# Kernel optimization log

Hardware: AMD Instinct MI355X
Metric: run time of the kernel (lower is better)

The kernel has to match this reference:

```python
import jax, jax.numpy as jnp
import numpy as np

HIDDEN = 1024
HEADS = 16
HEAD_DIM = HIDDEN // HEADS


def setup_inputs() -> dict:
    key = jax.random.key(0)
    ks = jax.random.split(key, 9)
    B, S = 2, 2048
    std = 1.0 / np.sqrt(HIDDEN)
    inp = {
        'hidden_states': jax.random.normal(ks[0], (B, S, HIDDEN), dtype=jnp.float32),
        'attention_mask': jnp.ones((B, S), dtype=jnp.int32),
        'wq': jax.random.normal(ks[1], (HIDDEN, HIDDEN), dtype=jnp.float32) * std,
        'bq': jnp.zeros((HIDDEN,), dtype=jnp.float32),
        'wk': jax.random.normal(ks[2], (HIDDEN, HIDDEN), dtype=jnp.float32) * std,
        'bk': jnp.zeros((HIDDEN,), dtype=jnp.float32),
        'wv': jax.random.normal(ks[3], (HIDDEN, HIDDEN), dtype=jnp.float32) * std,
        'bv': jnp.zeros((HIDDEN,), dtype=jnp.float32),
        'wo': jax.random.normal(ks[4], (HIDDEN, HIDDEN), dtype=jnp.float32) * std,
        'bo': jnp.zeros((HIDDEN,), dtype=jnp.float32),
    }
    return inp


def reference(hidden_states, attention_mask, wq, bq, wk, bk, wv, bv, wo, bo):
    B, S, H = hidden_states.shape
    def heads(x):  # [B,S,H] -> [B,nh,S,hd]
        return x.reshape(B, S, HEADS, HEAD_DIM).transpose(0, 2, 1, 3)
    q = heads(hidden_states @ wq + bq)
    k = heads(hidden_states @ wk + bk)
    v = heads(hidden_states @ wv + bv)
    scores = jnp.einsum('bhqd,bhkd->bhqk', q, k) / np.sqrt(HEAD_DIM).astype(np.float32)
    causal = jnp.tril(jnp.ones((S, S), dtype=bool))  # True = keep
    keep = causal[None, None] & (attention_mask[:, None, None, :] != 0)
    scores = jnp.where(keep, scores, -jnp.inf)
    probs = jax.nn.softmax(scores, axis=-1)
    out = jnp.einsum('bhqk,bhkd->bhqd', probs, v)  # [B,nh,S,hd]
    out = out.transpose(0, 2, 1, 3).reshape(B, S, H)
    return out @ wo + bo
```

## Files before the change

### kernel.cpp

```cpp
#include <hip/hip_runtime.h>

#define HID   1024
#define SLEN  2048
#define NHEAD 16
#define HDIM  64
#define SC2L  0.18033688f

typedef unsigned short u16;
typedef _Float16 f16;
using bf16x8 = __attribute__((ext_vector_type(8))) short;
using f16x4  = __attribute__((ext_vector_type(4))) f16;
using f32x4  = __attribute__((ext_vector_type(4))) float;

typedef __attribute__((address_space(1))) void gvoid;
typedef __attribute__((address_space(3))) void lvoid;

__device__ __forceinline__ u16 f2bf(float f) {
  union { float f; unsigned u; } v; v.f = f;
  unsigned u = v.u;
  return (u16)((u + 0x7fffu + ((u >> 16) & 1u)) >> 16);
}

__device__ __forceinline__ void async_ld16(const u16* g, u16* l) {
  __builtin_amdgcn_global_load_lds((gvoid*)g, (lvoid*)l, 16, 0, 0);
}

__global__ __launch_bounds__(256) void prep_kernel(const float* __restrict__ x,
                                                   const float* __restrict__ wq,
                                                   const float* __restrict__ wk,
                                                   const float* __restrict__ wv,
                                                   const float* __restrict__ wo,
                                                   u16* __restrict__ xb,
                                                   u16* __restrict__ wt) {
  const int tid = threadIdx.x;
  if (blockIdx.z == 4) {
    const int bid = blockIdx.y * 32 + blockIdx.x;
#pragma unroll
    for (int it = 0; it < 4; ++it) {
      const int i = bid * 1024 + it * 256 + tid;
      float4 v = ((const float4*)x)[i];
      ushort4 o;
      o.x = f2bf(v.x); o.y = f2bf(v.y); o.z = f2bf(v.z); o.w = f2bf(v.w);
      ((ushort4*)xb)[i] = o;
    }
    return;
  }
  const float* src = (blockIdx.z == 0) ? wq : (blockIdx.z == 1) ? wk
                   : (blockIdx.z == 2) ? wv : wo;
  u16* dst = wt + (size_t)blockIdx.z * (HID * HID);
  __shared__ float tile[32][33];
  const int n0 = blockIdx.x * 32, k0 = blockIdx.y * 32;
  const int xx = tid & 31, yy = tid >> 5;
  for (int i = yy; i < 32; i += 8)
    tile[i][xx] = src[(size_t)(k0 + i) * HID + n0 + xx];
  __syncthreads();
  for (int i = yy; i < 32; i += 8)
    dst[(size_t)(n0 + i) * HID + k0 + xx] = f2bf(tile[xx][i]);
}

__global__ __launch_bounds__(256) void gemm_qkv_kernel(const u16* __restrict__ A,
                                                       const u16* __restrict__ Bt,
                                                       const float* __restrict__ bq,
                                                       const float* __restrict__ bk,
                                                       const float* __restrict__ bv,
                                                       u16* __restrict__ Qb,
                                                       u16* __restrict__ Kb,
                                                       u16* __restrict__ VTf) {
  __shared__ u16 smem[8192];
  u16* sA = smem;
  u16* sB = smem + 4096;
  const int tid  = threadIdx.x;
  const int wave = tid >> 6, lane = tid & 63;
  const int quad = lane >> 4, l16 = lane & 15;
  const int n0g = blockIdx.x * 128;
  const int region = blockIdx.x >> 3;
  const int colbase = (blockIdx.x & 7) * 128;
  const int m0 = blockIdx.y * 128;
  const int wm = (wave & 1) * 64, wn = (wave >> 1) * 64;

  f32x4 acc[4][4] = {};
  const int srow = lane >> 2;
  const int scol = (lane & 3) * 8;

  for (int kt = 0; kt < HID; kt += 32) {
    __syncthreads();
    for (int c = wave; c < 8; c += 4) {
      async_ld16(A  + (size_t)(m0  + c * 16 + srow) * HID + kt + scol, &sA[c * 512]);
      async_ld16(Bt + (size_t)(n0g + c * 16 + srow) * HID + kt + scol, &sB[c * 512]);
    }
    __syncthreads();

    bf16x8 af[4], bfr[4];
#pragma unroll
    for (int t = 0; t < 4; ++t) {
      af[t]  = *(const bf16x8*)&sA[(wm + t * 16 + l16) * 32 + quad * 8];
      bfr[t] = *(const bf16x8*)&sB[(wn + t * 16 + l16) * 32 + quad * 8];
    }
#pragma unroll
    for (int mt = 0; mt < 4; ++mt)
#pragma unroll
      for (int nt = 0; nt < 4; ++nt)
        acc[mt][nt] = __builtin_amdgcn_mfma_f32_16x16x32_bf16(af[mt], bfr[nt],
                                                              acc[mt][nt], 0, 0, 0);
  }

  const float* bias = (region == 0) ? bq : (region == 1) ? bk : bv;
  float bvv[4];
#pragma unroll
  for (int nt = 0; nt < 4; ++nt) bvv[nt] = bias[colbase + wn + nt * 16 + l16];

  if (region == 2) {
    const int bb = m0 >> 11;
    const int m0loc = m0 & 2047;
    const int h0 = colbase >> 6;
    u16* T = smem;
#pragma unroll
    for (int h2 = 0; h2 < 2; ++h2) {
      __syncthreads();
      if ((wave >> 1) == h2) {
#pragma unroll
        for (int mt = 0; mt < 4; ++mt)
#pragma unroll
          for (int nt = 0; nt < 4; ++nt)
#pragma unroll
            for (int r = 0; r < 4; ++r) {
              const int sl = (wave & 1) * 64 + mt * 16 + quad * 4 + r;
              const int dl = nt * 16 + l16;
              union { f16 h; u16 u; } cv;
              cv.h = (f16)(acc[mt][nt][r] + bvv[nt]);
              T[dl * 128 + (((sl >> 3) ^ l16) * 8) + (sl & 7)] = cv.u;
            }
      }
      __syncthreads();
      const int d = tid >> 2, sg = (tid & 3) * 4;
      u16* drow = VTf + (size_t)((bb * NHEAD + h0 + h2) * HDIM + d) * SLEN + m0loc;
#pragma unroll
      for (int cc = 0; cc < 4; ++cc) {
        const int cl = sg + cc;
        const int ph = cl ^ (d & 15);
        *(bf16x8*)(drow + cl * 8) = *(const bf16x8*)&T[d * 128 + ph * 8];
      }
    }
    return;
  }

  u16* C = (region == 0) ? Qb : Kb;
#pragma unroll
  for (int mt = 0; mt < 4; ++mt)
#pragma unroll
    for (int r = 0; r < 4; ++r) {
      const int row = m0 + wm + mt * 16 + quad * 4 + r;
#pragma unroll
      for (int nt = 0; nt < 4; ++nt) {
        const int col = colbase + wn + nt * 16 + l16;
        C[(size_t)row * HID + col] = f2bf(acc[mt][nt][r] + bvv[nt]);
      }
    }
}

__global__ __launch_bounds__(256) void gemm_o_kernel(const u16* __restrict__ A,
                                                     const u16* __restrict__ Bt,
                                                     const float* __restrict__ bias,
                                                     float* __restrict__ Cf) {
  __shared__ u16 sA[64 * 32];
  __shared__ u16 sB[128 * 32];
  const int tid  = threadIdx.x;
  const int wave = tid >> 6, lane = tid & 63;
  const int quad = lane >> 4, l16 = lane & 15;
  const int n0 = blockIdx.x * 128;
  const int m0 = blockIdx.y * 64;
  const int wn = wave * 32;

  f32x4 acc[4][2] = {};
  const int srow = lane >> 2;
  const int scol = (lane & 3) * 8;

  for (int kt = 0; kt < HID; kt += 32) {
    __syncthreads();
    for (int c = wave; c < 12; c += 4) {
      if (c < 4) async_ld16(A  + (size_t)(m0 + c * 16 + srow) * HID + kt + scol, &sA[c * 512]);
      else       async_ld16(Bt + (size_t)(n0 + (c - 4) * 16 + srow) * HID + kt + scol,
                            &sB[(c - 4) * 512]);
    }
    __syncthreads();

    bf16x8 af[4], bfr[2];
#pragma unroll
    for (int t = 0; t < 4; ++t)
      af[t] = *(const bf16x8*)&sA[(t * 16 + l16) * 32 + quad * 8];
#pragma unroll
    for (int t = 0; t < 2; ++t)
      bfr[t] = *(const bf16x8*)&sB[(wn + t * 16 + l16) * 32 + quad * 8];
#pragma unroll
    for (int mt = 0; mt < 4; ++mt)
#pragma unroll
      for (int nt = 0; nt < 2; ++nt)
        acc[mt][nt] = __builtin_amdgcn_mfma_f32_16x16x32_bf16(af[mt], bfr[nt],
                                                              acc[mt][nt], 0, 0, 0);
  }

  float bvv[2];
#pragma unroll
  for (int nt = 0; nt < 2; ++nt) bvv[nt] = bias[n0 + wn + nt * 16 + l16];
#pragma unroll
  for (int mt = 0; mt < 4; ++mt)
#pragma unroll
    for (int r = 0; r < 4; ++r) {
      const int row = m0 + mt * 16 + quad * 4 + r;
#pragma unroll
      for (int nt = 0; nt < 2; ++nt)
        Cf[(size_t)row * HID + n0 + wn + nt * 16 + l16] = acc[mt][nt][r] + bvv[nt];
    }
}

__global__ __launch_bounds__(256, 2) void flash_attn_kernel(const u16* __restrict__ Q,
                                                            const u16* __restrict__ K,
                                                            const u16* __restrict__ VT,
                                                            const int* __restrict__ mask,
                                                            u16* __restrict__ O) {
  const int xb = blockIdx.x, h = blockIdx.y, b = blockIdx.z;
  const int tid  = threadIdx.x;
  const int wave = tid >> 6, lane = tid & 63;
  const int quad = lane >> 4, l16 = lane & 15;

  __shared__ alignas(16) char smraw[35840];
  u16*   Ks  = (u16*)smraw;
  u16*   Vt  = (u16*)(smraw + 16384);
  float* Ob0 = (float*)smraw;
  float* Ob1 = (float*)(smraw + 16896);
  float* lb  = (float*)(smraw + 33792);

  const u16* Kh  = K  + (size_t)b * SLEN * HID + h * HDIM;
  const u16* Vth = VT + (size_t)((b * NHEAD + h) * HDIM) * SLEN;

  const int srow8 = lane >> 3;
  const int gch   = (lane & 7) ^ srow8;
  const int rx    = l16 & 7;

  for (int phase = 0; phase < 2; ++phase) {
    const int qt = phase ? (31 - xb) : xb;
    const int q0 = qt * 64;

    bf16x8 qb[4][2];
#pragma unroll
    for (int nt = 0; nt < 4; ++nt) {
      const u16* qp = Q + (size_t)(b * SLEN + q0 + nt * 16 + l16) * HID + h * HDIM + quad * 8;
      qb[nt][0] = *(const bf16x8*)qp;
      qb[nt][1] = *(const bf16x8*)(qp + 32);
    }

    f32x4 oacc[4][4] = {};
    float l_part[4] = {0.f, 0.f, 0.f, 0.f};

    {
      const int r0 = wave * 16 + srow8;
      async_ld16(Kh  + (size_t)r0 * HID + gch * 8,        Ks + wave * 1024);
      async_ld16(Kh  + (size_t)(r0 + 8) * HID + gch * 8,  Ks + wave * 1024 + 512);
      async_ld16(Vth + (size_t)r0 * SLEN + gch * 8,       Vt + wave * 1024);
      async_ld16(Vth + (size_t)(r0 + 8) * SLEN + gch * 8, Vt + wave * 1024 + 512);
    }
    __syncthreads();

    for (int j = 0; j <= qt; ++j) {
      const int buf = j & 1;
      u16* KsB = Ks + buf * 4096;
      u16* VtB = Vt + buf * 4096;

      if (j < qt) {
        const int nb = (buf ^ 1) * 4096;
        const int jn = (j + 1) * 64;
        const int r0 = wave * 16 + srow8;
        async_ld16(Kh  + (size_t)(jn + r0) * HID + gch * 8,       Ks + nb + wave * 1024);
        async_ld16(Kh  + (size_t)(jn + r0 + 8) * HID + gch * 8,   Ks + nb + wave * 1024 + 512);
        async_ld16(Vth + (size_t)r0 * SLEN + jn + gch * 8,        Vt + nb + wave * 1024);
        async_ld16(Vth + (size_t)(r0 + 8) * SLEN + jn + gch * 8,  Vt + nb + wave * 1024 + 512);
      }

      const int4 mi = *(const int4*)(mask + b * SLEN + j * 64 + wave * 16 + quad * 4);
      float map[4];
      map[0] = mi.x ? 0.f : -1e30f;  map[1] = mi.y ? 0.f : -1e30f;
      map[2] = mi.z ? 0.f : -1e30f;  map[3] = mi.w ? 0.f : -1e30f;

      const u16* kp = KsB + (wave * 16 + l16) * 64;
      const int ph0 = quad ^ rx;
      const bf16x8 ka0 = *(const bf16x8*)(kp + ph0 * 8);
      const bf16x8 ka1 = *(const bf16x8*)(kp + (ph0 ^ 4) * 8);

      float p[4][4];
#pragma unroll
      for (int nt = 0; nt < 4; ++nt) {
        f32x4 z = {0.f, 0.f, 0.f, 0.f};
        z = __builtin_amdgcn_mfma_f32_16x16x32_bf16(ka0, qb[nt][0], z, 0, 0, 0);
        z = __builtin_amdgcn_mfma_f32_16x16x32_bf16(ka1, qb[nt][1], z, 0, 0, 0);
#pragma unroll
        for (int r = 0; r < 4; ++r)
          p[nt][r] = exp2f(fmaf(z[r], SC2L, map[r]));
      }
      if (j == qt) {
#pragma unroll
        for (int nt = 0; nt < 4; ++nt)
#pragma unroll
          for (int r = 0; r < 4; ++r)
            if (wave * 16 + quad * 4 + r > nt * 16 + l16) p[nt][r] = 0.f;
      }

      f16x4 pb[4];
#pragma unroll
      for (int nt = 0; nt < 4; ++nt) {
        l_part[nt] += (p[nt][0] + p[nt][1]) + (p[nt][2] + p[nt][3]);
        pb[nt][0] = (f16)p[nt][0]; pb[nt][1] = (f16)p[nt][1];
        pb[nt][2] = (f16)p[nt][2]; pb[nt][3] = (f16)p[nt][3];
      }

      const int phv = (wave * 2 + (quad >> 1)) ^ rx;
      const int vsub = phv * 8 + (quad & 1) * 4;
#pragma unroll
      for (int dt = 0; dt < 4; ++dt) {
        const f16x4 va = *(const f16x4*)(VtB + (dt * 16 + l16) * 64 + vsub);
#pragma unroll
        for (int nt = 0; nt < 4; ++nt)
          oacc[dt][nt] = __builtin_amdgcn_mfma_f32_16x16x16f16(va, pb[nt], oacc[dt][nt], 0, 0, 0);
      }
      __syncthreads();
    }

#pragma unroll
    for (int nt = 0; nt < 4; ++nt) {
      l_part[nt] += __shfl_xor(l_part[nt], 16);
      l_part[nt] += __shfl_xor(l_part[nt], 32);
    }
    if (quad == 0)
#pragma unroll
      for (int nt = 0; nt < 4; ++nt) lb[wave * 64 + nt * 16 + l16] = l_part[nt];

    if ((wave & 1) == 0) {
      float* ob = (wave == 0) ? Ob0 : Ob1;
#pragma unroll
      for (int dt = 0; dt < 4; ++dt)
#pragma unroll
        for (int nt = 0; nt < 4; ++nt)
#pragma unroll
          for (int r = 0; r < 4; ++r)
            ob[(dt * 16 + quad * 4 + r) * 66 + nt * 16 + l16] = oacc[dt][nt][r];
    }
    __syncthreads();
    if (wave & 1) {
      float* ob = (wave == 1) ? Ob0 : Ob1;
#pragma unroll
      for (int dt = 0; dt < 4; ++dt)
#pragma unroll
        for (int nt = 0; nt < 4; ++nt)
#pragma unroll
          for (int r = 0; r < 4; ++r)
            ob[(dt * 16 + quad * 4 + r) * 66 + nt * 16 + l16] += oacc[dt][nt][r];
    }
    __syncthreads();

    {
      const int q  = tid >> 2;
      const int dc = tid & 3;
      const float l = lb[q] + lb[64 + q] + lb[128 + q] + lb[192 + q];
      const float inv = 1.f / l;
      u16 ob[16];
#pragma unroll
      for (int e = 0; e < 16; ++e) {
        const int d = dc * 16 + e;
        ob[e] = f2bf((Ob0[d * 66 + q] + Ob1[d * 66 + q]) * inv);
      }
      u16* op = O + (size_t)(b * SLEN + q0 + q) * HID + h * HDIM + dc * 16;
      *(bf16x8*)op       = *(bf16x8*)&ob[0];
      *(bf16x8*)(op + 8) = *(bf16x8*)&ob[8];
    }
    __syncthreads();
  }
}

extern "C" void kernel_launch(void* const* d_in, const int* in_sizes, int n_in,
                              void* d_out, int out_size, void* d_ws, size_t ws_size,
                              hipStream_t stream) {
  const float* x    = (const float*)d_in[0];
  const int*   mask = (const int*)d_in[1];
  const float* wq   = (const float*)d_in[2];
  const float* bq   = (const float*)d_in[3];
  const float* wk   = (const float*)d_in[4];
  const float* bk   = (const float*)d_in[5];
  const float* wv   = (const float*)d_in[6];
  const float* bv   = (const float*)d_in[7];
  const float* wo   = (const float*)d_in[8];
  const float* bo   = (const float*)d_in[9];
  float* out = (float*)d_out;

  char* ws = (char*)d_ws;
  u16* XBF = (u16*)(ws);
  u16* WT  = (u16*)(ws + (8u  << 20));
  u16* QBF = (u16*)(ws + (16u << 20));
  u16* KBF = (u16*)(ws + (24u << 20));
  u16* VTF = (u16*)(ws + (32u << 20));
  u16* ATT = (u16*)(ws);

  prep_kernel<<<dim3(32, 32, 5), 256, 0, stream>>>(x, wq, wk, wv, wo, XBF, WT);
  gemm_qkv_kernel<<<dim3(24, 32), 256, 0, stream>>>(XBF, WT, bq, bk, bv, QBF, KBF, VTF);
  flash_attn_kernel<<<dim3(16, NHEAD, 2), 256, 0, stream>>>(QBF, KBF, VTF, mask, ATT);
  gemm_o_kernel<<<dim3(8, 64), 256, 0, stream>>>(ATT, WT + (3u << 20), bo, out);
}
```

Baseline: 208.7 us.

## Re-layout V^T into per-wave slabs and drop block barriers in attention loop

The V^T projection output is stored in contiguous 2KB slabs of 16 keys by 64 dims, with an XOR swizzle. This lets each wave async-load exactly the K and V rows it later consumes. Because no wave reads another wave's LDS tiles, the per-iteration __syncthreads is replaced by per-wave s_waitcnt vmcnt waits, and the next tile's mask load is prefetched. This removes cross-wave barrier stalls and gives more contiguous V loads. The cost is reliance on hand-placed waitcnt ordering for async LDS loads.

Result: faster. 199.2 us (-4.6%).

```diff
diff --git a/kernel.cpp b/kernel.cpp
--- a/kernel.cpp
+++ b/kernel.cpp
@@ -133,12 +133,14 @@
       }
       __syncthreads();
       const int d = tid >> 2, sg = (tid & 3) * 4;
-      u16* drow = VTf + (size_t)((bb * NHEAD + h0 + h2) * HDIM + d) * SLEN + m0loc;
+      u16* slab0 = VTf + ((size_t)((bb * NHEAD + h0 + h2) * 128 + (m0loc >> 4))) * 1024;
 #pragma unroll
       for (int cc = 0; cc < 4; ++cc) {
         const int cl = sg + cc;
         const int ph = cl ^ (d & 15);
-        *(bf16x8*)(drow + cl * 8) = *(const bf16x8*)&T[d * 128 + ph * 8];
+        const int slot = (d * 2 + (cl & 1)) ^ ((d >> 2) & 1);
+        *(bf16x8*)(slab0 + (size_t)(cl >> 1) * 1024 + slot * 8)
+            = *(const bf16x8*)&T[d * 128 + ph * 8];
       }
     }
     return;
@@ -231,7 +233,7 @@
   float* lb  = (float*)(smraw + 33792);
 
   const u16* Kh  = K  + (size_t)b * SLEN * HID + h * HDIM;
-  const u16* Vth = VT + (size_t)((b * NHEAD + h) * HDIM) * SLEN;
+  const u16* Vth = VT + (size_t)(b * NHEAD + h) * (128 * 1024);
 
   const int srow8 = lane >> 3;
   const int gch   = (lane & 7) ^ srow8;
@@ -254,29 +256,39 @@
 
     {
       const int r0 = wave * 16 + srow8;
-      async_ld16(Kh  + (size_t)r0 * HID + gch * 8,        Ks + wave * 1024);
-      async_ld16(Kh  + (size_t)(r0 + 8) * HID + gch * 8,  Ks + wave * 1024 + 512);
-      async_ld16(Vth + (size_t)r0 * SLEN + gch * 8,       Vt + wave * 1024);
-      async_ld16(Vth + (size_t)(r0 + 8) * SLEN + gch * 8, Vt + wave * 1024 + 512);
-    }
-    __syncthreads();
+      u16* kd = Ks + wave * 1024;
+      async_ld16(Kh + (size_t)r0 * HID + gch * 8,       kd);
+      async_ld16(Kh + (size_t)(r0 + 8) * HID + gch * 8, kd + 512);
+      const u16* vs = Vth + (size_t)wave * 1024;
+      u16* vd = Vt + wave * 1024;
+      async_ld16(vs + lane * 8,        vd);
+      async_ld16(vs + (64 + lane) * 8, vd + 512);
+    }
+    int4 mi = *(const int4*)(mask + b * SLEN + wave * 16 + quad * 4);
 
     for (int j = 0; j <= qt; ++j) {
       const int buf = j & 1;
       u16* KsB = Ks + buf * 4096;
       u16* VtB = Vt + buf * 4096;
 
+      int4 mi_n = mi;
       if (j < qt) {
         const int nb = (buf ^ 1) * 4096;
-        const int jn = (j + 1) * 64;
+        const int jn = j + 1;
         const int r0 = wave * 16 + srow8;
-        async_ld16(Kh  + (size_t)(jn + r0) * HID + gch * 8,       Ks + nb + wave * 1024);
-        async_ld16(Kh  + (size_t)(jn + r0 + 8) * HID + gch * 8,   Ks + nb + wave * 1024 + 512);
-        async_ld16(Vth + (size_t)r0 * SLEN + jn + gch * 8,        Vt + nb + wave * 1024);
-        async_ld16(Vth + (size_t)(r0 + 8) * SLEN + jn + gch * 8,  Vt + nb + wave * 1024 + 512);
-      }
-
-      const int4 mi = *(const int4*)(mask + b * SLEN + j * 64 + wave * 16 + quad * 4);
+        u16* kd = Ks + nb + wave * 1024;
+        async_ld16(Kh + (size_t)(jn * 64 + r0) * HID + gch * 8,     kd);
+        async_ld16(Kh + (size_t)(jn * 64 + r0 + 8) * HID + gch * 8, kd + 512);
+        const u16* vs = Vth + (size_t)(jn * 4 + wave) * 1024;
+        u16* vd = Vt + nb + wave * 1024;
+        async_ld16(vs + lane * 8,        vd);
+        async_ld16(vs + (64 + lane) * 8, vd + 512);
+        asm volatile("s_waitcnt vmcnt(4)" ::: "memory");
+        mi_n = *(const int4*)(mask + b * SLEN + jn * 64 + wave * 16 + quad * 4);
+      } else {
+        asm volatile("s_waitcnt vmcnt(0)" ::: "memory");
+      }
+
       float map[4];
       map[0] = mi.x ? 0.f : -1e30f;  map[1] = mi.y ? 0.f : -1e30f;
       map[2] = mi.z ? 0.f : -1e30f;  map[3] = mi.w ? 0.f : -1e30f;
@@ -312,17 +324,19 @@
         pb[nt][2] = (f16)p[nt][2]; pb[nt][3] = (f16)p[nt][3];
       }
 
-      const int phv = (wave * 2 + (quad >> 1)) ^ rx;
-      const int vsub = phv * 8 + (quad & 1) * 4;
 #pragma unroll
       for (int dt = 0; dt < 4; ++dt) {
-        const f16x4 va = *(const f16x4*)(VtB + (dt * 16 + l16) * 64 + vsub);
+        const int dd = dt * 16 + l16;
+        const int slot = (dd * 2 + (quad >> 1)) ^ ((dd >> 2) & 1);
+        const f16x4 va = *(const f16x4*)(VtB + wave * 1024 + slot * 8 + (quad & 1) * 4);
 #pragma unroll
         for (int nt = 0; nt < 4; ++nt)
           oacc[dt][nt] = __builtin_amdgcn_mfma_f32_16x16x16f16(va, pb[nt], oacc[dt][nt], 0, 0, 0);
       }
-      __syncthreads();
-    }
+      mi = mi_n;
+    }
+
+    __syncthreads();
 
 #pragma unroll
     for (int nt = 0; nt < 4; ++nt) {
```
